# Optimization experiments

Hardware: AMD Instinct MI355X
Metric: run time of the kernel (lower is better)

The kernel has to match this reference:

```python
import jax, jax.numpy as jnp
import numpy as np

NEG_SLOPE = 0.2  # PyG GATConv default LeakyReLU negative slope
NUM_GRAPHS = 256


def gat_conv(x, edge_src, edge_dst, W, att_src, att_dst, bias):
    """PyG-style GATConv. x:[N,Fin], W:[H*C,Fin], att_*:[H,C], bias:[H*C]."""
    N = x.shape[0]
    H, C = att_src.shape
    h = (x @ W.T).reshape(N, H, C)                       # [N,H,C]
    a_src = jnp.sum(h * att_src, axis=-1)                # [N,H]
    a_dst = jnp.sum(h * att_dst, axis=-1)                # [N,H]
    e = jax.nn.leaky_relu(a_src[edge_src] + a_dst[edge_dst], NEG_SLOPE)  # [E,H]
    # segment softmax over edges sharing the same destination node
    m = jax.ops.segment_max(e, edge_dst, num_segments=N)
    ex = jnp.exp(e - m[edge_dst])
    den = jax.ops.segment_sum(ex, edge_dst, num_segments=N)
    alpha = ex / (den[edge_dst] + 1e-16)                 # [E,H]
    out = jax.ops.segment_sum(h[edge_src] * alpha[..., None], edge_dst,
                              num_segments=N)            # [N,H,C]
    return out.reshape(N, H * C) + bias


def setup_inputs() -> dict:
    key = jax.random.key(0)
    ks = jax.random.split(key, 16)
    N, E, Fin = 20000, 320000, 128
    H1, C1 = 8, 64          # conv1: heads=8, hidden_dim1=64 -> concat 512
    D1 = H1 * C1            # 512
    D2 = 128                # hidden_dim2, conv2 heads=1
    OUT = 2
    s = lambda k, shp, fan: jax.random.normal(k, shp, jnp.float32) * (1.0 / np.sqrt(fan))
    x = jax.random.normal(ks[0], (N, Fin), jnp.float32)
    edge_index = jax.random.randint(ks[1], (2, E), 0, N, jnp.int32)
    batch = jnp.sort(jax.random.randint(ks[2], (N,), 0, NUM_GRAPHS, jnp.int32))
    return {
        "x": x, "edge_index": edge_index, "batch": batch,
        "W1": s(ks[3], (D1, Fin), Fin), "att_src1": s(ks[4], (H1, C1), C1),
        "att_dst1": s(ks[5], (H1, C1), C1), "b1": jnp.zeros((D1,), jnp.float32),
        "W2": s(ks[6], (D2, D1), D1), "att_src2": s(ks[7], (1, D2), D2),
        "att_dst2": s(ks[8], (1, D2), D2), "b2": jnp.zeros((D2,), jnp.float32),
        "w_attn": s(ks[9], (D2, 1), D2), "b_attn": jnp.zeros((1,), jnp.float32),
        "w_mask": s(ks[10], (D2, 1), D2), "b_mask": jnp.zeros((1,), jnp.float32),
        "W_out": s(ks[11], (OUT, D2), D2), "b_out": jnp.zeros((OUT,), jnp.float32),
    }


def reference(x, edge_index, batch, W1, att_src1, att_dst1, b1,
              W2, att_src2, att_dst2, b2, w_attn, b_attn, w_mask, b_mask,
              W_out, b_out):
    N = x.shape[0]
    loops = jnp.arange(N, dtype=edge_index.dtype)
    src = jnp.concatenate([edge_index[0], loops])  # PyG add_self_loops=True
    dst = jnp.concatenate([edge_index[1], loops])

    h = gat_conv(x, src, dst, W1, att_src1, att_dst1, b1)   # [N, 512]
    h = jax.nn.relu(h)                                      # dropout = identity (eval)
    h = gat_conv(h, src, dst, W2, att_src2, att_dst2, b2)   # [N, 128]
    h = jax.nn.relu(h)

    # attention pooling over graphs in the batch
    attn_scores = h @ w_attn + b_attn                       # [N,1]
    node_mask = jax.nn.sigmoid(h @ w_mask + b_mask)         # [N,1]
    weighted = h * (attn_scores * node_mask)                # [N,128]
    pooled = jax.ops.segment_sum(weighted, batch, num_segments=NUM_GRAPHS)
    return pooled @ W_out.T + b_out                         # [256, 2]
```

## Files before the change

### kernel.cpp

```cpp
#include <hip/hip_runtime.h>
#include <math.h>


#define NEG_SLOPE 0.2f

using bf16x8 = __attribute__((ext_vector_type(8))) __bf16;
using f32x4  = __attribute__((ext_vector_type(4))) float;

__device__ __forceinline__ ushort f2bf(float f) {
    unsigned u = __float_as_uint(f);
    unsigned r = (u + 0x7FFFu + ((u >> 16) & 1u)) >> 16;
    return (ushort)r;
}
__device__ __forceinline__ unsigned pack2(float a, float b) {
    return (unsigned)f2bf(a) | ((unsigned)f2bf(b) << 16);
}
__device__ __forceinline__ void unpack8(uint4 u, float* f) {
    f[0] = __uint_as_float(u.x << 16); f[1] = __uint_as_float(u.x & 0xFFFF0000u);
    f[2] = __uint_as_float(u.y << 16); f[3] = __uint_as_float(u.y & 0xFFFF0000u);
    f[4] = __uint_as_float(u.z << 16); f[5] = __uint_as_float(u.z & 0xFFFF0000u);
    f[6] = __uint_as_float(u.w << 16); f[7] = __uint_as_float(u.w & 0xFFFF0000u);
}

__device__ __forceinline__ float leaky(float e) {
    return e > 0.f ? e : NEG_SLOPE * e;
}

__global__ __launch_bounds__(256) void cvt_bf16(const float* __restrict__ in,
                                                ushort* __restrict__ out, int n4) {
    int i = blockIdx.x * 256 + threadIdx.x;
    if (i >= n4) return;
    float4 v = ((const float4*)in)[i];
    uint2 o;
    o.x = pack2(v.x, v.y);
    o.y = pack2(v.z, v.w);
    ((uint2*)out)[i] = o;
}

__global__ __launch_bounds__(256) void prep_v(const float* __restrict__ W1,
                                              const float* __restrict__ att_s,
                                              const float* __restrict__ att_d,
                                              float* __restrict__ v_s,
                                              float* __restrict__ v_d) {
    int tid = blockIdx.x * 256 + threadIdx.x;
    int h = tid >> 7, f = tid & 127;
    float as = 0.f, ad = 0.f;
    for (int c = 0; c < 64; ++c) {
        float w = W1[(size_t)(h * 64 + c) * 128 + f];
        as += att_s[h * 64 + c] * w;
        ad += att_d[h * 64 + c] * w;
    }
    v_s[tid] = as;
    v_d[tid] = ad;
}

__global__ __launch_bounds__(256) void scoresA(const ushort* __restrict__ xb,
                                               const float* __restrict__ v_s,
                                               const float* __restrict__ v_d,
                                               float* __restrict__ a1s,
                                               float* __restrict__ a1d, int N) {
    int node = blockIdx.x * 4 + (threadIdx.x >> 6);
    if (node >= N) return;
    int lane = threadIdx.x & 63;
    int head = lane >> 3, f0 = (lane & 7) * 16;
    const uint4* xp = (const uint4*)(xb + (size_t)node * 128 + f0);
    float xv[16];
    unpack8(xp[0], xv);
    unpack8(xp[1], xv + 8);
    const float4* sp = (const float4*)(v_s + head * 128 + f0);
    const float4* dp = (const float4*)(v_d + head * 128 + f0);
    float ps = 0.f, pd = 0.f;
#pragma unroll
    for (int q = 0; q < 4; ++q) {
        float4 s4 = sp[q], d4 = dp[q];
        ps += xv[q*4+0]*s4.x + xv[q*4+1]*s4.y + xv[q*4+2]*s4.z + xv[q*4+3]*s4.w;
        pd += xv[q*4+0]*d4.x + xv[q*4+1]*d4.y + xv[q*4+2]*d4.z + xv[q*4+3]*d4.w;
    }
#pragma unroll
    for (int off = 1; off < 8; off <<= 1) {
        ps += __shfl_xor(ps, off);
        pd += __shfl_xor(pd, off);
    }
    if ((lane & 7) == 0) {
        a1s[node * 8 + head] = ps;
        a1d[node * 8 + head] = pd;
    }
}

__global__ void count_edges(const int* __restrict__ dst, int* cnt, int E) {
    int e = blockIdx.x * 256 + threadIdx.x;
    if (e < E) atomicAdd(&cnt[dst[e]], 1);
}

__global__ __launch_bounds__(1024) void scan_offsets(const int* cnt, int* row_start,
                                                     int* cursor, int N) {
    __shared__ int sm[1024];
    int t = threadIdx.x;
    int per = (N + 1023) / 1024;
    int beg = t * per;
    int end = beg + per; if (end > N) end = N;
    int sum = 0;
    for (int i = beg; i < end; ++i) sum += cnt[i];
    sm[t] = sum;
    __syncthreads();
    for (int off = 1; off < 1024; off <<= 1) {
        int add = (t >= off) ? sm[t - off] : 0;
        __syncthreads();
        sm[t] += add;
        __syncthreads();
    }
    int run = sm[t] - sum;
    for (int i = beg; i < end; ++i) {
        int c = cnt[i];
        row_start[i] = run;
        cursor[i] = run;
        run += c;
    }
    if (t == 1023) row_start[N] = run;
}

__global__ void fill_edges(const int* __restrict__ src, const int* __restrict__ dst,
                           int* cursor, int* __restrict__ srcs,
                           int* __restrict__ dsts, int E) {
    int e = blockIdx.x * 256 + threadIdx.x;
    if (e < E) {
        int d = dst[e];
        int pos = atomicAdd(&cursor[d], 1);
        srcs[pos] = src[e];
        dsts[pos] = d;
    }
}

__global__ __launch_bounds__(256) void exp_edges1(const int* __restrict__ srcs,
                                                  const int* __restrict__ dsts,
                                                  const float* __restrict__ a1s,
                                                  const float* __restrict__ a1d,
                                                  float* __restrict__ ex1, int E) {
    int p = blockIdx.x * 256 + threadIdx.x;
    if (p >= E) return;
    int s = srcs[p], d = dsts[p];
    const float4* sp = (const float4*)(a1s + s * 8);
    const float4* dp = (const float4*)(a1d + d * 8);
    float4 s0 = sp[0], s1 = sp[1], d0 = dp[0], d1 = dp[1];
    float4 o0, o1;
    o0.x = __expf(leaky(s0.x + d0.x));
    o0.y = __expf(leaky(s0.y + d0.y));
    o0.z = __expf(leaky(s0.z + d0.z));
    o0.w = __expf(leaky(s0.w + d0.w));
    o1.x = __expf(leaky(s1.x + d1.x));
    o1.y = __expf(leaky(s1.y + d1.y));
    o1.z = __expf(leaky(s1.z + d1.z));
    o1.w = __expf(leaky(s1.w + d1.w));
    float4* op = (float4*)(ex1 + (size_t)p * 8);
    op[0] = o0; op[1] = o1;
}

__global__ __launch_bounds__(256) void exp_edges2(const int* __restrict__ srcs,
                                                  const int* __restrict__ dsts,
                                                  const float* __restrict__ a2s,
                                                  const float* __restrict__ a2d,
                                                  float* __restrict__ ex2, int E) {
    int p = blockIdx.x * 256 + threadIdx.x;
    if (p >= E) return;
    ex2[p] = __expf(leaky(a2s[srcs[p]] + a2d[dsts[p]]));
}

__global__ __launch_bounds__(256) void agg_x(const ushort* __restrict__ xb,
                                             const float* __restrict__ a1s,
                                             const float* __restrict__ a1d,
                                             const int* __restrict__ row_start,
                                             const int* __restrict__ srcs,
                                             const float* __restrict__ ex1,
                                             ushort* __restrict__ ax, int N) {
    int node = blockIdx.x;
    if (node >= N) return;
    int hp = threadIdx.x >> 6;
    int lane = threadIdx.x & 63;
    int eg = lane >> 4, fl = lane & 15;
    int f0 = fl * 8;
    int pbeg = row_start[node], pend = row_start[node + 1];
    float acc0[8] = {}, acc1[8] = {};
    float den0 = 0.f, den1 = 0.f;
    for (int p = pbeg + eg; p < pend; p += 4) {
        int s = srcs[p];
        float2 e2 = *(const float2*)(ex1 + (size_t)p * 8 + hp * 2);
        float xv[8];
        unpack8(*(const uint4*)(xb + (size_t)s * 128 + f0), xv);
        den0 += e2.x;
        den1 += e2.y;
#pragma unroll
        for (int j = 0; j < 8; ++j) {
            acc0[j] += e2.x * xv[j];
            acc1[j] += e2.y * xv[j];
        }
    }
    den0 += __shfl_xor(den0, 16); den0 += __shfl_xor(den0, 32);
    den1 += __shfl_xor(den1, 16); den1 += __shfl_xor(den1, 32);
#pragma unroll
    for (int j = 0; j < 8; ++j) {
        acc0[j] += __shfl_xor(acc0[j], 16); acc0[j] += __shfl_xor(acc0[j], 32);
        acc1[j] += __shfl_xor(acc1[j], 16); acc1[j] += __shfl_xor(acc1[j], 32);
    }
    {
        float2 sv = *(const float2*)(a1s + node * 8 + hp * 2);
        float2 dv = *(const float2*)(a1d + node * 8 + hp * 2);
        float e0 = __expf(leaky(sv.x + dv.x));
        float e1 = __expf(leaky(sv.y + dv.y));
        float xv[8];
        unpack8(*(const uint4*)(xb + (size_t)node * 128 + f0), xv);
        den0 += e0;
        den1 += e1;
#pragma unroll
        for (int j = 0; j < 8; ++j) {
            acc0[j] += e0 * xv[j];
            acc1[j] += e1 * xv[j];
        }
    }
    if (eg < 2) {
        float den = (eg == 0) ? den0 : den1;
        float rden = 1.0f / (den + 1e-16f);
        float v[8];
#pragma unroll
        for (int j = 0; j < 8; ++j)
            v[j] = ((eg == 0) ? acc0[j] : acc1[j]) * rden;
        uint4 o;
        o.x = pack2(v[0], v[1]);
        o.y = pack2(v[2], v[3]);
        o.z = pack2(v[4], v[5]);
        o.w = pack2(v[6], v[7]);
        *(uint4*)(ax + (size_t)node * 1024 + (2 * hp + eg) * 128 + f0) = o;
    }
}

#define LDSB 40
__global__ __launch_bounds__(256) void gemm_grouped(const ushort* __restrict__ AX,
                                                    const ushort* __restrict__ W1b,
                                                    const float* __restrict__ b1,
                                                    ushort* __restrict__ r1,
                                                    int M) {
    __shared__ ushort As[2][128 * LDSB];
    __shared__ ushort Bs[128 * LDSB];
    int t = threadIdx.x;
    int wave = t >> 6, lane = t & 63;
    int quad = lane >> 4, l16 = lane & 15;
    int m0 = blockIdx.x * 128;
    int y = blockIdx.y;
    int wm = (wave & 1) * 64;
    int wn = (wave >> 1) * 64;
    int hsel = wn >> 6;
    int srow = t >> 1;
    int sseg = (t & 1) * 16;
    f32x4 acc[4][4] = {};
    for (int k0 = 0; k0 < 128; k0 += 32) {
        uint4 a0v0, a0v1, a1v0, a1v1, bv0, bv1;
        {
            int grow = m0 + srow;
            if (grow < M) {
                const uint4* g0 = (const uint4*)(AX + (size_t)grow * 1024 + (2 * y) * 128 + k0 + sseg);
                const uint4* g1 = (const uint4*)(AX + (size_t)grow * 1024 + (2 * y + 1) * 128 + k0 + sseg);
                a0v0 = g0[0]; a0v1 = g0[1];
                a1v0 = g1[0]; a1v1 = g1[1];
            } else {
                a0v0 = make_uint4(0, 0, 0, 0); a0v1 = a0v0; a1v0 = a0v0; a1v1 = a0v0;
            }
            const uint4* gq = (const uint4*)(W1b + (size_t)(y * 128 + srow) * 128 + k0 + sseg);
            bv0 = gq[0]; bv1 = gq[1];
        }
        __syncthreads();
        *(uint4*)&As[0][srow * LDSB + sseg]     = a0v0;
        *(uint4*)&As[0][srow * LDSB + sseg + 8] = a0v1;
        *(uint4*)&As[1][srow * LDSB + sseg]     = a1v0;
        *(uint4*)&As[1][srow * LDSB + sseg + 8] = a1v1;
        *(uint4*)&Bs[srow * LDSB + sseg]        = bv0;
        *(uint4*)&Bs[srow * LDSB + sseg + 8]    = bv1;
        __syncthreads();
        bf16x8 af[4], bf[4];
#pragma unroll
        for (int i = 0; i < 4; ++i)
            af[i] = *(const bf16x8*)&As[hsel][(wm + i * 16 + l16) * LDSB + quad * 8];
#pragma unroll
        for (int j = 0; j < 4; ++j)
            bf[j] = *(const bf16x8*)&Bs[(wn + j * 16 + l16) * LDSB + quad * 8];
#pragma unroll
        for (int i = 0; i < 4; ++i)
#pragma unroll
            for (int j = 0; j < 4; ++j)
                acc[i][j] = __builtin_amdgcn_mfma_f32_16x16x32_bf16(
                    af[i], bf[j], acc[i][j], 0, 0, 0);
    }
#pragma unroll
    for (int i = 0; i < 4; ++i) {
#pragma unroll
        for (int r = 0; r < 4; ++r) {
            int grow = m0 + wm + i * 16 + quad * 4 + r;
            if (grow < M) {
#pragma unroll
                for (int j = 0; j < 4; ++j) {
                    int gcol = y * 128 + wn + j * 16 + l16;
                    float v = fmaxf(acc[i][j][r] + b1[gcol], 0.f);
                    r1[(size_t)grow * 512 + gcol] = f2bf(v);
                }
            }
        }
    }
}

__global__ __launch_bounds__(256) void gemm_mfma(const ushort* __restrict__ A,
                                                 const ushort* __restrict__ B,
                                                 ushort* __restrict__ C,
                                                 int M, int N, int K) {
    __shared__ ushort As[128 * LDSB];
    __shared__ ushort Bs[128 * LDSB];
    int t = threadIdx.x;
    int wave = t >> 6, lane = t & 63;
    int quad = lane >> 4, l16 = lane & 15;
    int m0 = blockIdx.x * 128;
    int n0 = blockIdx.y * 128;
    int wm = (wave & 1) * 64;
    int wn = (wave >> 1) * 64;
    int srow = t >> 1;
    int sseg = (t & 1) * 16;
    f32x4 acc[4][4] = {};
    for (int k0 = 0; k0 < K; k0 += 32) {
        uint4 av0, av1, bv0, bv1;
        {
            int grow = m0 + srow;
            if (grow < M) {
                const uint4* gp = (const uint4*)(A + (size_t)grow * K + k0 + sseg);
                av0 = gp[0]; av1 = gp[1];
            } else {
                av0 = make_uint4(0, 0, 0, 0); av1 = av0;
            }
            const uint4* gq = (const uint4*)(B + (size_t)(n0 + srow) * K + k0 + sseg);
            bv0 = gq[0]; bv1 = gq[1];
        }
        __syncthreads();
        *(uint4*)&As[srow * LDSB + sseg]     = av0;
        *(uint4*)&As[srow * LDSB + sseg + 8] = av1;
        *(uint4*)&Bs[srow * LDSB + sseg]     = bv0;
        *(uint4*)&Bs[srow * LDSB + sseg + 8] = bv1;
        __syncthreads();
        bf16x8 af[4], bf[4];
#pragma unroll
        for (int i = 0; i < 4; ++i)
            af[i] = *(const bf16x8*)&As[(wm + i * 16 + l16) * LDSB + quad * 8];
#pragma unroll
        for (int j = 0; j < 4; ++j)
            bf[j] = *(const bf16x8*)&Bs[(wn + j * 16 + l16) * LDSB + quad * 8];
#pragma unroll
        for (int i = 0; i < 4; ++i)
#pragma unroll
            for (int j = 0; j < 4; ++j)
                acc[i][j] = __builtin_amdgcn_mfma_f32_16x16x32_bf16(
                    af[i], bf[j], acc[i][j], 0, 0, 0);
    }
#pragma unroll
    for (int i = 0; i < 4; ++i) {
#pragma unroll
        for (int r = 0; r < 4; ++r) {
            int grow = m0 + wm + i * 16 + quad * 4 + r;
            if (grow < M) {
#pragma unroll
                for (int j = 0; j < 4; ++j) {
                    int gcol = n0 + wn + j * 16 + l16;
                    C[(size_t)grow * N + gcol] = f2bf(acc[i][j][r]);
                }
            }
        }
    }
}

__global__ __launch_bounds__(256) void scores2(const ushort* __restrict__ h2,
                                               const float* __restrict__ att_s,
                                               const float* __restrict__ att_d,
                                               float* __restrict__ a2s,
                                               float* __restrict__ a2d, int N) {
    int node = blockIdx.x * 4 + (threadIdx.x >> 6);
    if (node >= N) return;
    int lane = threadIdx.x & 63;
    unsigned u = *(const unsigned*)(h2 + (size_t)node * 128 + lane * 2);
    float h0 = __uint_as_float(u << 16), h1v = __uint_as_float(u & 0xFFFF0000u);
    float2 s = *(const float2*)(att_s + lane * 2);
    float2 d = *(const float2*)(att_d + lane * 2);
    float ps = h0 * s.x + h1v * s.y;
    float pd = h0 * d.x + h1v * d.y;
#pragma unroll
    for (int off = 1; off < 64; off <<= 1) {
        ps += __shfl_xor(ps, off);
        pd += __shfl_xor(pd, off);
    }
    if (lane == 0) { a2s[node] = ps; a2d[node] = pd; }
}

__global__ __launch_bounds__(256) void agg2(const ushort* __restrict__ h2,
                                            const float* __restrict__ a2s,
                                            const float* __restrict__ a2d,
                                            const int* __restrict__ row_start,
                                            const int* __restrict__ srcs,
                                            const float* __restrict__ ex2,
                                            const float* __restrict__ b2,
                                            const float* __restrict__ w_attn,
                                            const float* __restrict__ b_attn,
                                            const float* __restrict__ w_mask,
                                            const float* __restrict__ b_mask,
                                            float* __restrict__ wh, int N) {
    int node = blockIdx.x * 4 + (threadIdx.x >> 6);
    if (node >= N) return;
    int lane = threadIdx.x & 63;
    int eg = lane >> 4, fl = lane & 15;
    int f0 = fl * 8;
    int pbeg = row_start[node], pend = row_start[node + 1];
    float acc[8] = {};
    float den = 0.f;
    for (int p = pbeg + eg; p < pend; p += 4) {
        int s = srcs[p];
        float ex = ex2[p];
        float v[8];
        unpack8(*(const uint4*)(h2 + (size_t)s * 128 + f0), v);
        den += ex;
#pragma unroll
        for (int j = 0; j < 8; ++j) acc[j] += ex * v[j];
    }
    den += __shfl_xor(den, 16);
    den += __shfl_xor(den, 32);
#pragma unroll
    for (int j = 0; j < 8; ++j) {
        acc[j] += __shfl_xor(acc[j], 16);
        acc[j] += __shfl_xor(acc[j], 32);
    }
    {
        float exs = __expf(leaky(a2s[node] + a2d[node]));
        float q[8];
        unpack8(*(const uint4*)(h2 + (size_t)node * 128 + f0), q);
        den += exs;
#pragma unroll
        for (int j = 0; j < 8; ++j) acc[j] += exs * q[j];
    }
    float rden = 1.0f / (den + 1e-16f);
    const float4* bp = (const float4*)(b2 + f0);
    float4 b0 = bp[0], b1v = bp[1];
    float o[8];
    o[0] = fmaxf(acc[0] * rden + b0.x, 0.f);
    o[1] = fmaxf(acc[1] * rden + b0.y, 0.f);
    o[2] = fmaxf(acc[2] * rden + b0.z, 0.f);
    o[3] = fmaxf(acc[3] * rden + b0.w, 0.f);
    o[4] = fmaxf(acc[4] * rden + b1v.x, 0.f);
    o[5] = fmaxf(acc[5] * rden + b1v.y, 0.f);
    o[6] = fmaxf(acc[6] * rden + b1v.z, 0.f);
    o[7] = fmaxf(acc[7] * rden + b1v.w, 0.f);
    const float4* wap = (const float4*)(w_attn + f0);
    const float4* wmp = (const float4*)(w_mask + f0);
    float4 wa0 = wap[0], wa1 = wap[1], wm0 = wmp[0], wm1 = wmp[1];
    float pa = o[0]*wa0.x + o[1]*wa0.y + o[2]*wa0.z + o[3]*wa0.w +
               o[4]*wa1.x + o[5]*wa1.y + o[6]*wa1.z + o[7]*wa1.w;
    float pm = o[0]*wm0.x + o[1]*wm0.y + o[2]*wm0.z + o[3]*wm0.w +
               o[4]*wm1.x + o[5]*wm1.y + o[6]*wm1.z + o[7]*wm1.w;
#pragma unroll
    for (int off = 1; off < 16; off <<= 1) {
        pa += __shfl_xor(pa, off);
        pm += __shfl_xor(pm, off);
    }
    float attn = pa + b_attn[0];
    float mask = 1.0f / (1.0f + __expf(-(pm + b_mask[0])));
    float w = attn * mask;
    if (eg == 0) {
        float* pp = wh + (size_t)node * 128 + f0;
        float4 o0 = make_float4(o[0] * w, o[1] * w, o[2] * w, o[3] * w);
        float4 o1 = make_float4(o[4] * w, o[5] * w, o[6] * w, o[7] * w);
        *(float4*)(pp)     = o0;
        *(float4*)(pp + 4) = o1;
    }
}

__global__ __launch_bounds__(128) void pool_seg(const float* __restrict__ wh,
                                                const int* __restrict__ batch,
                                                const float* __restrict__ W_out,
                                                const float* __restrict__ b_out,
                                                float* __restrict__ out, int N) {
    int g = blockIdx.x;
    int t = threadIdx.x;
    int lo = 0, hi = N;
    while (lo < hi) { int mid = (lo + hi) >> 1; if (batch[mid] < g) lo = mid + 1; else hi = mid; }
    int beg = lo;
    hi = N;
    while (lo < hi) { int mid = (lo + hi) >> 1; if (batch[mid] <= g) lo = mid + 1; else hi = mid; }
    int end = lo;
    float s = 0.f;
    for (int r = beg; r < end; ++r) s += wh[(size_t)r * 128 + t];
    __shared__ float sm[128];
    sm[t] = s;
    __syncthreads();
    if (t < 2) {
        const float* w = W_out + t * 128;
        float acc = 0.f;
#pragma unroll 4
        for (int f = 0; f < 128; ++f) acc += sm[f] * w[f];
        out[g * 2 + t] = acc + b_out[t];
    }
}

extern "C" void kernel_launch(void* const* d_in, const int* in_sizes, int n_in,
                              void* d_out, int out_size, void* d_ws, size_t ws_size,
                              hipStream_t stream) {
    const float* x        = (const float*)d_in[0];
    const int* edge_index = (const int*)d_in[1];
    const int* batch      = (const int*)d_in[2];
    const float* W1       = (const float*)d_in[3];
    const float* att_src1 = (const float*)d_in[4];
    const float* att_dst1 = (const float*)d_in[5];
    const float* b1       = (const float*)d_in[6];
    const float* W2       = (const float*)d_in[7];
    const float* att_src2 = (const float*)d_in[8];
    const float* att_dst2 = (const float*)d_in[9];
    const float* b2       = (const float*)d_in[10];
    const float* w_attn   = (const float*)d_in[11];
    const float* b_attn   = (const float*)d_in[12];
    const float* w_mask   = (const float*)d_in[13];
    const float* b_mask   = (const float*)d_in[14];
    const float* W_out    = (const float*)d_in[15];
    const float* b_out    = (const float*)d_in[16];
    float* out = (float*)d_out;

    int N = in_sizes[0] / 128;
    int E = in_sizes[1] / 2;
    const int* esrc = edge_index;
    const int* edst = edge_index + E;

    char* ws = (char*)d_ws;
    size_t off = 0;
    auto alloc = [&](size_t bytes) {
        void* p = ws + off;
        off = (off + bytes + 255) & ~(size_t)255;
        return p;
    };
    ushort* xb       = (ushort*)alloc((size_t)N * 128 * 2);
    ushort* ax       = (ushort*)alloc((size_t)N * 1024 * 2);
    ushort* r1       = (ushort*)alloc((size_t)N * 512 * 2);
    ushort* h2       = (ushort*)alloc((size_t)N * 128 * 2);
    float*  wh       = (float*)alloc((size_t)N * 128 * 4);
    ushort* w1b      = (ushort*)alloc((size_t)512 * 128 * 2);
    ushort* w2b      = (ushort*)alloc((size_t)128 * 512 * 2);
    float*  v_s      = (float*)alloc((size_t)8 * 128 * 4);
    float*  v_d      = (float*)alloc((size_t)8 * 128 * 4);
    float*  a1s      = (float*)alloc((size_t)N * 8 * 4);
    float*  a1d      = (float*)alloc((size_t)N * 8 * 4);
    float*  a2s      = (float*)alloc((size_t)N * 4);
    float*  a2d      = (float*)alloc((size_t)N * 4);
    int*    row_start= (int*)alloc((size_t)(N + 1) * 4);
    int*    cursor   = (int*)alloc((size_t)N * 4);
    int*    srcs     = (int*)alloc((size_t)E * 4);
    int*    dsts     = (int*)alloc((size_t)E * 4);
    float*  ex1      = (float*)alloc((size_t)E * 8 * 4);
    float*  ex2      = (float*)alloc((size_t)E * 4);

    hipMemsetAsync(cursor, 0, (size_t)N * 4, stream);

    dim3 b256(256);
    int nx4 = N * 128 / 4;
    cvt_bf16<<<(nx4 + 255) / 256, b256, 0, stream>>>(x, xb, nx4);
    cvt_bf16<<<(512 * 128 / 4 + 255) / 256, b256, 0, stream>>>(W1, w1b, 512 * 128 / 4);
    cvt_bf16<<<(128 * 512 / 4 + 255) / 256, b256, 0, stream>>>(W2, w2b, 128 * 512 / 4);
    prep_v<<<4, b256, 0, stream>>>(W1, att_src1, att_dst1, v_s, v_d);
    scoresA<<<(N + 3) / 4, b256, 0, stream>>>(xb, v_s, v_d, a1s, a1d, N);
    count_edges<<<(E + 255) / 256, b256, 0, stream>>>(edst, cursor, E);
    scan_offsets<<<1, 1024, 0, stream>>>(cursor, row_start, cursor, N);
    fill_edges<<<(E + 255) / 256, b256, 0, stream>>>(esrc, edst, cursor, srcs, dsts, E);
    exp_edges1<<<(E + 255) / 256, b256, 0, stream>>>(srcs, dsts, a1s, a1d, ex1, E);
    agg_x<<<N, b256, 0, stream>>>(xb, a1s, a1d, row_start, srcs, ex1, ax, N);
    gemm_grouped<<<dim3((N + 127) / 128, 4), b256, 0, stream>>>(ax, w1b, b1, r1, N);
    gemm_mfma<<<dim3((N + 127) / 128, 1), b256, 0, stream>>>(r1, w2b, h2, N, 128, 512);
    scores2<<<(N + 3) / 4, b256, 0, stream>>>(h2, att_src2, att_dst2, a2s, a2d, N);
    exp_edges2<<<(E + 255) / 256, b256, 0, stream>>>(srcs, dsts, a2s, a2d, ex2, E);
    agg2<<<(N + 3) / 4, b256, 0, stream>>>(h2, a2s, a2d, row_start, srcs, ex2, b2,
                                           w_attn, b_attn, w_mask, b_mask, wh, N);
    pool_seg<<<256, 128, 0, stream>>>(wh, batch, W_out, b_out, out, N);
}
```

Before: 336.3 us.

## Drop x bf16 conversion, parallelize CSR scan, split layer-1 denominator from aggregation

Result: faster. 324.0 us (-3.6%).

```diff
diff --git a/kernel.cpp b/kernel.cpp
--- a/kernel.cpp
+++ b/kernel.cpp
@@ -26,15 +26,21 @@
     return e > 0.f ? e : NEG_SLOPE * e;
 }
 
-__global__ __launch_bounds__(256) void cvt_bf16(const float* __restrict__ in,
-                                                ushort* __restrict__ out, int n4) {
+__global__ __launch_bounds__(256) void cvt_w(const float* __restrict__ W1,
+                                             const float* __restrict__ W2,
+                                             ushort* __restrict__ w1b,
+                                             ushort* __restrict__ w2b) {
     int i = blockIdx.x * 256 + threadIdx.x;
-    if (i >= n4) return;
-    float4 v = ((const float4*)in)[i];
+    const float* src;
+    ushort* dst;
+    int j;
+    if (i < 16384) { src = W1; dst = w1b; j = i; }
+    else           { src = W2; dst = w2b; j = i - 16384; }
+    float4 v = ((const float4*)src)[j];
     uint2 o;
     o.x = pack2(v.x, v.y);
     o.y = pack2(v.z, v.w);
-    ((uint2*)out)[i] = o;
+    ((uint2*)dst)[j] = o;
 }
 
 __global__ __launch_bounds__(256) void prep_v(const float* __restrict__ W1,
@@ -54,7 +60,7 @@
     v_d[tid] = ad;
 }
 
-__global__ __launch_bounds__(256) void scoresA(const ushort* __restrict__ xb,
+__global__ __launch_bounds__(256) void scoresA(const float* __restrict__ x,
                                                const float* __restrict__ v_s,
                                                const float* __restrict__ v_d,
                                                float* __restrict__ a1s,
@@ -63,18 +69,15 @@
     if (node >= N) return;
     int lane = threadIdx.x & 63;
     int head = lane >> 3, f0 = (lane & 7) * 16;
-    const uint4* xp = (const uint4*)(xb + (size_t)node * 128 + f0);
-    float xv[16];
-    unpack8(xp[0], xv);
-    unpack8(xp[1], xv + 8);
+    const float4* xp = (const float4*)(x + (size_t)node * 128 + f0);
     const float4* sp = (const float4*)(v_s + head * 128 + f0);
     const float4* dp = (const float4*)(v_d + head * 128 + f0);
     float ps = 0.f, pd = 0.f;
 #pragma unroll
     for (int q = 0; q < 4; ++q) {
-        float4 s4 = sp[q], d4 = dp[q];
-        ps += xv[q*4+0]*s4.x + xv[q*4+1]*s4.y + xv[q*4+2]*s4.z + xv[q*4+3]*s4.w;
-        pd += xv[q*4+0]*d4.x + xv[q*4+1]*d4.y + xv[q*4+2]*d4.z + xv[q*4+3]*d4.w;
+        float4 xv = xp[q], s4 = sp[q], d4 = dp[q];
+        ps += xv.x * s4.x + xv.y * s4.y + xv.z * s4.z + xv.w * s4.w;
+        pd += xv.x * d4.x + xv.y * d4.y + xv.z * d4.z + xv.w * d4.w;
     }
 #pragma unroll
     for (int off = 1; off < 8; off <<= 1) {
@@ -92,31 +95,57 @@
     if (e < E) atomicAdd(&cnt[dst[e]], 1);
 }
 
-__global__ __launch_bounds__(1024) void scan_offsets(const int* cnt, int* row_start,
-                                                     int* cursor, int N) {
-    __shared__ int sm[1024];
+__global__ __launch_bounds__(128) void scan_p1(const int* __restrict__ cnt,
+                                               int* __restrict__ partial, int N) {
+    int i = blockIdx.x * 128 + threadIdx.x;
+    int v = (i < N) ? cnt[i] : 0;
+#pragma unroll
+    for (int off = 1; off < 64; off <<= 1) v += __shfl_xor(v, off);
+    __shared__ int sm[2];
+    if ((threadIdx.x & 63) == 0) sm[threadIdx.x >> 6] = v;
+    __syncthreads();
+    if (threadIdx.x == 0) partial[blockIdx.x] = sm[0] + sm[1];
+}
+
+__global__ __launch_bounds__(256) void scan_p2(int* __restrict__ partial,
+                                               int* __restrict__ row_start,
+                                               int nb, int N, int E) {
+    __shared__ int sm[256];
     int t = threadIdx.x;
-    int per = (N + 1023) / 1024;
-    int beg = t * per;
-    int end = beg + per; if (end > N) end = N;
-    int sum = 0;
-    for (int i = beg; i < end; ++i) sum += cnt[i];
-    sm[t] = sum;
+    int v = (t < nb) ? partial[t] : 0;
+    sm[t] = v;
     __syncthreads();
-    for (int off = 1; off < 1024; off <<= 1) {
+    for (int off = 1; off < 256; off <<= 1) {
         int add = (t >= off) ? sm[t - off] : 0;
         __syncthreads();
         sm[t] += add;
         __syncthreads();
     }
-    int run = sm[t] - sum;
-    for (int i = beg; i < end; ++i) {
-        int c = cnt[i];
-        row_start[i] = run;
-        cursor[i] = run;
-        run += c;
-    }
-    if (t == 1023) row_start[N] = run;
+    if (t < nb) partial[t] = sm[t] - v;
+    if (t == 0) row_start[N] = E;
+}
+
+__global__ __launch_bounds__(128) void scan_p3(const int* __restrict__ cnt,
+                                               const int* __restrict__ partial,
+                                               int* __restrict__ row_start,
+                                               int* __restrict__ cursor, int N) {
+    __shared__ int sm[128];
+    int i = blockIdx.x * 128 + threadIdx.x;
+    int t = threadIdx.x;
+    int v = (i < N) ? cnt[i] : 0;
+    sm[t] = v;
+    __syncthreads();
+    for (int off = 1; off < 128; off <<= 1) {
+        int add = (t >= off) ? sm[t - off] : 0;
+        __syncthreads();
+        sm[t] += add;
+        __syncthreads();
+    }
+    if (i < N) {
+        int start = partial[blockIdx.x] + sm[t] - v;
+        row_start[i] = start;
+        cursor[i] = start;
+    }
 }
 
 __global__ void fill_edges(const int* __restrict__ src, const int* __restrict__ dst,
@@ -165,70 +194,90 @@
     ex2[p] = __expf(leaky(a2s[srcs[p]] + a2d[dsts[p]]));
 }
 
-__global__ __launch_bounds__(256) void agg_x(const ushort* __restrict__ xb,
+__global__ __launch_bounds__(256) void den1_kernel(const float* __restrict__ ex1,
+                                                   const float* __restrict__ a1s,
+                                                   const float* __restrict__ a1d,
+                                                   const int* __restrict__ row_start,
+                                                   float* __restrict__ den, int N) {
+    int node = blockIdx.x * 4 + (threadIdx.x >> 6);
+    if (node >= N) return;
+    int lane = threadIdx.x & 63;
+    int s = lane >> 3, h = lane & 7;
+    int pbeg = row_start[node], pend = row_start[node + 1];
+    float d = 0.f;
+    for (int p = pbeg + s; p < pend; p += 8) d += ex1[(size_t)p * 8 + h];
+    d += __shfl_xor(d, 8);
+    d += __shfl_xor(d, 16);
+    d += __shfl_xor(d, 32);
+    if (s == 0) {
+        float e = __expf(leaky(a1s[node * 8 + h] + a1d[node * 8 + h]));
+        den[node * 8 + h] = d + e;
+    }
+}
+
+__global__ __launch_bounds__(256) void agg_x(const float* __restrict__ x,
                                              const float* __restrict__ a1s,
                                              const float* __restrict__ a1d,
+                                             const float* __restrict__ den,
                                              const int* __restrict__ row_start,
                                              const int* __restrict__ srcs,
                                              const float* __restrict__ ex1,
                                              ushort* __restrict__ ax, int N) {
     int node = blockIdx.x;
     if (node >= N) return;
-    int hp = threadIdx.x >> 6;
+    int w = threadIdx.x >> 6;
     int lane = threadIdx.x & 63;
     int eg = lane >> 4, fl = lane & 15;
-    int f0 = fl * 8;
+    int f = w * 32 + fl * 2;
     int pbeg = row_start[node], pend = row_start[node + 1];
-    float acc0[8] = {}, acc1[8] = {};
-    float den0 = 0.f, den1 = 0.f;
+    float acc[8][2] = {};
     for (int p = pbeg + eg; p < pend; p += 4) {
         int s = srcs[p];
-        float2 e2 = *(const float2*)(ex1 + (size_t)p * 8 + hp * 2);
-        float xv[8];
-        unpack8(*(const uint4*)(xb + (size_t)s * 128 + f0), xv);
-        den0 += e2.x;
-        den1 += e2.y;
-#pragma unroll
-        for (int j = 0; j < 8; ++j) {
-            acc0[j] += e2.x * xv[j];
-            acc1[j] += e2.y * xv[j];
+        const float4* ep = (const float4*)(ex1 + (size_t)p * 8);
+        float4 e0 = ep[0], e1 = ep[1];
+        float2 xv = *(const float2*)(x + (size_t)s * 128 + f);
+        acc[0][0] += e0.x * xv.x; acc[0][1] += e0.x * xv.y;
+        acc[1][0] += e0.y * xv.x; acc[1][1] += e0.y * xv.y;
+        acc[2][0] += e0.z * xv.x; acc[2][1] += e0.z * xv.y;
+        acc[3][0] += e0.w * xv.x; acc[3][1] += e0.w * xv.y;
+        acc[4][0] += e1.x * xv.x; acc[4][1] += e1.x * xv.y;
+        acc[5][0] += e1.y * xv.x; acc[5][1] += e1.y * xv.y;
+        acc[6][0] += e1.z * xv.x; acc[6][1] += e1.z * xv.y;
+        acc[7][0] += e1.w * xv.x; acc[7][1] += e1.w * xv.y;
+    }
+#pragma unroll
+    for (int h = 0; h < 8; ++h) {
+#pragma unroll
+        for (int j = 0; j < 2; ++j) {
+            acc[h][j] += __shfl_xor(acc[h][j], 16);
+            acc[h][j] += __shfl_xor(acc[h][j], 32);
         }
     }
-    den0 += __shfl_xor(den0, 16); den0 += __shfl_xor(den0, 32);
-    den1 += __shfl_xor(den1, 16); den1 += __shfl_xor(den1, 32);
-#pragma unroll
-    for (int j = 0; j < 8; ++j) {
-        acc0[j] += __shfl_xor(acc0[j], 16); acc0[j] += __shfl_xor(acc0[j], 32);
-        acc1[j] += __shfl_xor(acc1[j], 16); acc1[j] += __shfl_xor(acc1[j], 32);
-    }
-    {
-        float2 sv = *(const float2*)(a1s + node * 8 + hp * 2);
-        float2 dv = *(const float2*)(a1d + node * 8 + hp * 2);
-        float e0 = __expf(leaky(sv.x + dv.x));
-        float e1 = __expf(leaky(sv.y + dv.y));
-        float xv[8];
-        unpack8(*(const uint4*)(xb + (size_t)node * 128 + f0), xv);
-        den0 += e0;
-        den1 += e1;
-#pragma unroll
-        for (int j = 0; j < 8; ++j) {
-            acc0[j] += e0 * xv[j];
-            acc1[j] += e1 * xv[j];
+    if (eg == 0) {
+        const float4* sp = (const float4*)(a1s + node * 8);
+        const float4* dp = (const float4*)(a1d + node * 8);
+        float4 s0 = sp[0], s1 = sp[1], d0 = dp[0], d1 = dp[1];
+        float es[8];
+        es[0] = __expf(leaky(s0.x + d0.x));
+        es[1] = __expf(leaky(s0.y + d0.y));
+        es[2] = __expf(leaky(s0.z + d0.z));
+        es[3] = __expf(leaky(s0.w + d0.w));
+        es[4] = __expf(leaky(s1.x + d1.x));
+        es[5] = __expf(leaky(s1.y + d1.y));
+        es[6] = __expf(leaky(s1.z + d1.z));
+        es[7] = __expf(leaky(s1.w + d1.w));
+        float2 xv = *(const float2*)(x + (size_t)node * 128 + f);
+        const float4* dnp = (const float4*)(den + node * 8);
+        float4 dn0 = dnp[0], dn1 = dnp[1];
+        float dn[8] = {dn0.x, dn0.y, dn0.z, dn0.w, dn1.x, dn1.y, dn1.z, dn1.w};
+        ushort* base = ax + (size_t)node * 1024 + f;
+#pragma unroll
+        for (int h = 0; h < 8; ++h) {
+            float rden = 1.0f / (dn[h] + 1e-16f);
+            float v0 = (acc[h][0] + es[h] * xv.x) * rden;
+            float v1 = (acc[h][1] + es[h] * xv.y) * rden;
+            *(unsigned*)(base + h * 128) = pack2(v0, v1);
         }
-    }
-    if (eg < 2) {
-        float den = (eg == 0) ? den0 : den1;
-        float rden = 1.0f / (den + 1e-16f);
-        float v[8];
-#pragma unroll
-        for (int j = 0; j < 8; ++j)
-            v[j] = ((eg == 0) ? acc0[j] : acc1[j]) * rden;
-        uint4 o;
-        o.x = pack2(v[0], v[1]);
-        o.y = pack2(v[2], v[3]);
-        o.z = pack2(v[4], v[5]);
-        o.w = pack2(v[6], v[7]);
-        *(uint4*)(ax + (size_t)node * 1024 + (2 * hp + eg) * 128 + f0) = o;
     }
 }
 
@@ -465,10 +514,8 @@
     float w = attn * mask;
     if (eg == 0) {
         float* pp = wh + (size_t)node * 128 + f0;
-        float4 o0 = make_float4(o[0] * w, o[1] * w, o[2] * w, o[3] * w);
-        float4 o1 = make_float4(o[4] * w, o[5] * w, o[6] * w, o[7] * w);
-        *(float4*)(pp)     = o0;
-        *(float4*)(pp + 4) = o1;
+        *(float4*)(pp)     = make_float4(o[0] * w, o[1] * w, o[2] * w, o[3] * w);
+        *(float4*)(pp + 4) = make_float4(o[4] * w, o[5] * w, o[6] * w, o[7] * w);
     }
 }
 
@@ -533,7 +580,6 @@
         off = (off + bytes + 255) & ~(size_t)255;
         return p;
     };
-    ushort* xb       = (ushort*)alloc((size_t)N * 128 * 2);
     ushort* ax       = (ushort*)alloc((size_t)N * 1024 * 2);
     ushort* r1       = (ushort*)alloc((size_t)N * 512 * 2);
     ushort* h2       = (ushort*)alloc((size_t)N * 128 * 2);
@@ -544,10 +590,12 @@
     float*  v_d      = (float*)alloc((size_t)8 * 128 * 4);
     float*  a1s      = (float*)alloc((size_t)N * 8 * 4);
     float*  a1d      = (float*)alloc((size_t)N * 8 * 4);
+    float*  den      = (float*)alloc((size_t)N * 8 * 4);
     float*  a2s      = (float*)alloc((size_t)N * 4);
     float*  a2d      = (float*)alloc((size_t)N * 4);
     int*    row_start= (int*)alloc((size_t)(N + 1) * 4);
     int*    cursor   = (int*)alloc((size_t)N * 4);
+    int*    partial  = (int*)alloc((size_t)256 * 4);
     int*    srcs     = (int*)alloc((size_t)E * 4);
     int*    dsts     = (int*)alloc((size_t)E * 4);
     float*  ex1      = (float*)alloc((size_t)E * 8 * 4);
@@ -556,17 +604,18 @@
     hipMemsetAsync(cursor, 0, (size_t)N * 4, stream);
 
     dim3 b256(256);
-    int nx4 = N * 128 / 4;
-    cvt_bf16<<<(nx4 + 255) / 256, b256, 0, stream>>>(x, xb, nx4);
-    cvt_bf16<<<(512 * 128 / 4 + 255) / 256, b256, 0, stream>>>(W1, w1b, 512 * 128 / 4);
-    cvt_bf16<<<(128 * 512 / 4 + 255) / 256, b256, 0, stream>>>(W2, w2b, 128 * 512 / 4);
+    int nb = (N + 127) / 128;
+    cvt_w<<<128, b256, 0, stream>>>(W1, W2, w1b, w2b);
     prep_v<<<4, b256, 0, stream>>>(W1, att_src1, att_dst1, v_s, v_d);
-    scoresA<<<(N + 3) / 4, b256, 0, stream>>>(xb, v_s, v_d, a1s, a1d, N);
+    scoresA<<<(N + 3) / 4, b256, 0, stream>>>(x, v_s, v_d, a1s, a1d, N);
     count_edges<<<(E + 255) / 256, b256, 0, stream>>>(edst, cursor, E);
-    scan_offsets<<<1, 1024, 0, stream>>>(cursor, row_start, cursor, N);
+    scan_p1<<<nb, 128, 0, stream>>>(cursor, partial, N);
+    scan_p2<<<1, 256, 0, stream>>>(partial, row_start, nb, N, E);
+    scan_p3<<<nb, 128, 0, stream>>>(cursor, partial, row_start, cursor, N);
     fill_edges<<<(E + 255) / 256, b256, 0, stream>>>(esrc, edst, cursor, srcs, dsts, E);
     exp_edges1<<<(E + 255) / 256, b256, 0, stream>>>(srcs, dsts, a1s, a1d, ex1, E);
-    agg_x<<<N, b256, 0, stream>>>(xb, a1s, a1d, row_start, srcs, ex1, ax, N);
+    den1_kernel<<<(N + 3) / 4, b256, 0, stream>>>(ex1, a1s, a1d, row_start, den, N);
+    agg_x<<<N, b256, 0, stream>>>(x, a1s, a1d, den, row_start, srcs, ex1, ax, N);
     gemm_grouped<<<dim3((N + 127) / 128, 4), b256, 0, stream>>>(ax, w1b, b1, r1, N);
     gemm_mfma<<<dim3((N + 127) / 128, 1), b256, 0, stream>>>(r1, w2b, h2, N, 128, 512);
     scores2<<<(N + 3) / 4, b256, 0, stream>>>(h2, att_src2, att_dst2, a2s, a2d, N);
```
